# Kernel optimization log

Hardware: AMD Instinct MI355X
Metric: run time of the kernel (lower is better)

## Reference

```python
import jax, jax.numpy as jnp
import numpy as np

TAU = 1.0
LOSS_WEIGHT = 1.0
N = 4_000_000


def setup_inputs() -> dict:
    key = jax.random.key(0)
    k1, k2 = jax.random.split(key)

    def make_boxes(k):
        u = jax.random.uniform(k, (N, 5), dtype=jnp.float32)
        xy = u[:, :2] * 1024.0                 # centers in a 1024px image
        wh = u[:, 2:4] * 100.0 + 4.0           # box sizes in [4, 104)
        r = (u[:, 4:5] - 0.5) * jnp.pi         # angle in [-pi/2, pi/2)
        return jnp.concatenate([xy, wh, r], axis=-1)

    return {"pred": make_boxes(k1), "target": make_boxes(k2)}


def xy_wh_r_2_xy_sigma(xywhr):
    """(N,5) rbox -> (mu (N,2), sigma (N,2,2)) via R @ (S/2)^2 @ R^T closed form."""
    xy = xywhr[..., :2]
    wh = jnp.clip(xywhr[..., 2:4], 1e-7, 1e7)
    r = xywhr[..., 4]
    c, s = jnp.cos(r), jnp.sin(r)
    a = (0.5 * wh[..., 0]) ** 2  # (w/2)^2
    b = (0.5 * wh[..., 1]) ** 2  # (h/2)^2
    s00 = a * c * c + b * s * s
    s11 = a * s * s + b * c * c
    s01 = (a - b) * s * c
    sigma = jnp.stack(
        [jnp.stack([s00, s01], -1), jnp.stack([s01, s11], -1)], -2
    )  # (N,2,2)
    return xy, sigma


def _det2(m):
    return m[..., 0, 0] * m[..., 1, 1] - m[..., 0, 1] * m[..., 1, 0]


def _inv2(m):
    det = _det2(m)
    adj = jnp.stack(
        [jnp.stack([m[..., 1, 1], -m[..., 0, 1]], -1),
         jnp.stack([-m[..., 1, 0], m[..., 0, 0]], -1)], -2)
    return adj / det[..., None, None]


def kld_loss(mu_p, sigma_p, mu_t, sigma_t, tau):
    delta = mu_p - mu_t                                # (N,2)
    sigma_t_inv = _inv2(sigma_t)                       # (N,2,2)
    # delta^T Sigma_t^{-1} delta
    term1 = jnp.einsum('ni,nij,nj->n', delta, sigma_t_inv, delta)
    # tr(Sigma_t^{-1} Sigma_p) + log(det Sigma_t / det Sigma_p)
    tr = jnp.einsum('nij,nji->n', sigma_t_inv, sigma_p)
    term2 = tr + jnp.log(_det2(sigma_t) / _det2(sigma_p))
    dis = term1 + term2 - 2.0
    kl_dis = jnp.maximum(dis, 1e-6)
    # fun == 'log1p'
    loss = 1.0 - 1.0 / (tau + jnp.log1p(kl_dis))
    return loss[:, None]                               # (N,1) like torch version


def reference(pred, target):
    mu_p, sigma_p = xy_wh_r_2_xy_sigma(pred)
    mu_t, sigma_t = xy_wh_r_2_xy_sigma(target)
    return kld_loss(mu_p, sigma_p, mu_t, sigma_t, TAU) * LOSS_WEIGHT
```

## Files before the change

### kernel.cpp

```cpp
#include <hip/hip_runtime.h>
#include <math.h>

#define TAU_CONST 1.0f
#define BLOCK 256
#define RPT 4
#define RPB (BLOCK * RPT)
#define F4PB (RPB * 5 / 4)

__device__ __forceinline__ float fast_rcp(float x) { return __builtin_amdgcn_rcpf(x); }

__device__ __forceinline__ float kld_row(const float* p, const float* t) {
    float pw = fminf(fmaxf(p[2], 1e-7f), 1e7f), ph = fminf(fmaxf(p[3], 1e-7f), 1e7f);
    float tw = fminf(fmaxf(t[2], 1e-7f), 1e7f), th = fminf(fmaxf(t[3], 1e-7f), 1e7f);
    float ap = 0.25f * pw * pw, bp = 0.25f * ph * ph;
    float at = 0.25f * tw * tw, bt = 0.25f * th * th;
    float sp_, cp_; __sincosf(p[4], &sp_, &cp_);
    float st_, ct_; __sincosf(t[4], &st_, &ct_);
    float p00 = ap * cp_ * cp_ + bp * sp_ * sp_;
    float p11 = ap * sp_ * sp_ + bp * cp_ * cp_;
    float p01 = (ap - bp) * sp_ * cp_;
    float t00 = at * ct_ * ct_ + bt * st_ * st_;
    float t11 = at * st_ * st_ + bt * ct_ * ct_;
    float t01 = (at - bt) * st_ * ct_;
    float dp = p00 * p11 - p01 * p01;
    float dt = t00 * t11 - t01 * t01;
    float dx = p[0] - t[0], dy = p[1] - t[1];
    float inv_dt = fast_rcp(dt);
    float term1 = (dx * dx * t11 - 2.0f * dx * dy * t01 + dy * dy * t00) * inv_dt;
    float tr    = (t11 * p00 + t00 * p11 - 2.0f * t01 * p01) * inv_dt;
    float term2 = tr + (__logf(dt) - __logf(dp));
    float dis = term1 + term2 - 2.0f;
    float kl = fmaxf(dis, 1e-6f);
    return 1.0f - fast_rcp(TAU_CONST + __logf(1.0f + kl));
}

__global__ void __launch_bounds__(BLOCK) gdloss_lds_kernel(const float4* __restrict__ pred4,
                                                           const float4* __restrict__ targ4,
                                                           float4* __restrict__ out4,
                                                           int nf4_in, int n4_out) {
    __shared__ float4 sP[F4PB];
    __shared__ float4 sT[F4PB];
    const int tid = threadIdx.x;
    const int base4 = blockIdx.x * F4PB;
#pragma unroll
    for (int k = 0; k < 5; ++k) {
        int g = base4 + k * BLOCK + tid;
        float4 v, u;
        if (g < nf4_in) { v = pred4[g]; u = targ4[g]; }
        else            { v = float4{0, 0, 0, 0}; u = float4{0, 0, 0, 0}; }
        sP[k * BLOCK + tid] = v;
        sT[k * BLOCK + tid] = u;
    }
    __syncthreads();
    const float4* pRow = (const float4*)((const float*)sP + 20 * tid);
    const float4* tRow = (const float4*)((const float*)sT + 20 * tid);
    float4 lp[5], lt[5];
#pragma unroll
    for (int k = 0; k < 5; ++k) { lp[k] = pRow[k]; lt[k] = tRow[k]; }
    const float* P = (const float*)lp;
    const float* T = (const float*)lt;
    float4 o;
    o.x = kld_row(P + 0,  T + 0);
    o.y = kld_row(P + 5,  T + 5);
    o.z = kld_row(P + 10, T + 10);
    o.w = kld_row(P + 15, T + 15);
    int o4 = blockIdx.x * BLOCK + tid;
    if (o4 < n4_out) out4[o4] = o;
}

__global__ void gdloss_tail_kernel(const float* __restrict__ pred,
                                   const float* __restrict__ target,
                                   float* __restrict__ out, int start, int n) {
    int i = start + blockIdx.x * blockDim.x + threadIdx.x;
    if (i >= n) return;
    float p[5], t[5];
#pragma unroll
    for (int k = 0; k < 5; ++k) { p[k] = pred[5 * i + k]; t[k] = target[5 * i + k]; }
    out[i] = kld_row(p, t);
}

extern "C" void kernel_launch(void* const* d_in, const int* in_sizes, int n_in,
                              void* d_out, int out_size, void* d_ws, size_t ws_size,
                              hipStream_t stream) {
    const float* pred   = (const float*)d_in[0];
    const float* target = (const float*)d_in[1];
    float* out = (float*)d_out;
    const int n = in_sizes[0] / 5;
    const int n4 = n / 4;
    const int nf4_in = (n * 5) / 4;
    if (n4 > 0) {
        int blocks = (n4 + BLOCK - 1) / BLOCK;
        gdloss_lds_kernel<<<blocks, BLOCK, 0, stream>>>((const float4*)pred,
                                                        (const float4*)target,
                                                        (float4*)out, nf4_in, n4);
    }
    if (n - n4 * 4 > 0) {
        gdloss_tail_kernel<<<1, 64, 0, stream>>>(pred, target, out, n4 * 4, n);
    }
}
```

Baseline: 179.6 us.

## Replace LDS-staged kernel with grid-stride double-buffered register pipeline

Drops the shared-memory staging. Each thread now loads its own 4 rows (5 uncoalesced float4 per input) straight into registers. A persistent grid of at most 1024 blocks strides over the data and prefetches the next tile while computing the current one. Loads and stores use nontemporal hints. The direct per-thread loads stride 80 bytes across lanes, which loses coalescing, and the double buffers raise register pressure.

Result: slower. 194.4 us (+8.2%).

```diff
diff --git a/kernel.cpp b/kernel.cpp
--- a/kernel.cpp
+++ b/kernel.cpp
@@ -3,9 +3,9 @@
 
 #define TAU_CONST 1.0f
 #define BLOCK 256
-#define RPT 4
-#define RPB (BLOCK * RPT)
-#define F4PB (RPB * 5 / 4)
+#define NBLOCKS 1024
+
+typedef float vfloat4 __attribute__((ext_vector_type(4)));
 
 __device__ __forceinline__ float fast_rcp(float x) { return __builtin_amdgcn_rcpf(x); }
 
@@ -34,38 +34,63 @@
     return 1.0f - fast_rcp(TAU_CONST + __logf(1.0f + kl));
 }
 
-__global__ void __launch_bounds__(BLOCK) gdloss_lds_kernel(const float4* __restrict__ pred4,
-                                                           const float4* __restrict__ targ4,
-                                                           float4* __restrict__ out4,
-                                                           int nf4_in, int n4_out) {
-    __shared__ float4 sP[F4PB];
-    __shared__ float4 sT[F4PB];
-    const int tid = threadIdx.x;
-    const int base4 = blockIdx.x * F4PB;
+__device__ __forceinline__ void load_tile(const vfloat4* __restrict__ p4,
+                                          const vfloat4* __restrict__ t4,
+                                          int i, vfloat4* P, vfloat4* T) {
+    const long b = 5L * i;
 #pragma unroll
     for (int k = 0; k < 5; ++k) {
-        int g = base4 + k * BLOCK + tid;
-        float4 v, u;
-        if (g < nf4_in) { v = pred4[g]; u = targ4[g]; }
-        else            { v = float4{0, 0, 0, 0}; u = float4{0, 0, 0, 0}; }
-        sP[k * BLOCK + tid] = v;
-        sT[k * BLOCK + tid] = u;
+        P[k] = __builtin_nontemporal_load(p4 + b + k);
+        T[k] = __builtin_nontemporal_load(t4 + b + k);
     }
-    __syncthreads();
-    const float4* pRow = (const float4*)((const float*)sP + 20 * tid);
-    const float4* tRow = (const float4*)((const float*)sT + 20 * tid);
-    float4 lp[5], lt[5];
-#pragma unroll
-    for (int k = 0; k < 5; ++k) { lp[k] = pRow[k]; lt[k] = tRow[k]; }
-    const float* P = (const float*)lp;
-    const float* T = (const float*)lt;
-    float4 o;
-    o.x = kld_row(P + 0,  T + 0);
-    o.y = kld_row(P + 5,  T + 5);
-    o.z = kld_row(P + 10, T + 10);
-    o.w = kld_row(P + 15, T + 15);
-    int o4 = blockIdx.x * BLOCK + tid;
-    if (o4 < n4_out) out4[o4] = o;
+}
+
+__global__ void __launch_bounds__(BLOCK) gdloss_pipe_kernel(const vfloat4* __restrict__ pred4,
+                                                            const vfloat4* __restrict__ targ4,
+                                                            vfloat4* __restrict__ out4,
+                                                            int n4) {
+    const int stride = gridDim.x * blockDim.x;
+    int i = blockIdx.x * blockDim.x + threadIdx.x;
+    if (i >= n4) return;
+
+    vfloat4 Pa[5], Ta[5], Pb[5], Tb[5];
+    load_tile(pred4, targ4, i, Pa, Ta);
+
+    while (true) {
+        const int inext = i + stride;
+        const bool more = (inext < n4);
+        if (more) load_tile(pred4, targ4, inext, Pb, Tb);
+
+        {
+            const float* P = (const float*)Pa;
+            const float* T = (const float*)Ta;
+            vfloat4 o;
+            o.x = kld_row(P + 0,  T + 0);
+            o.y = kld_row(P + 5,  T + 5);
+            o.z = kld_row(P + 10, T + 10);
+            o.w = kld_row(P + 15, T + 15);
+            __builtin_nontemporal_store(o, out4 + i);
+        }
+        if (!more) break;
+        i = inext;
+
+        const int inext2 = i + stride;
+        const bool more2 = (inext2 < n4);
+        if (more2) load_tile(pred4, targ4, inext2, Pa, Ta);
+
+        {
+            const float* P = (const float*)Pb;
+            const float* T = (const float*)Tb;
+            vfloat4 o;
+            o.x = kld_row(P + 0,  T + 0);
+            o.y = kld_row(P + 5,  T + 5);
+            o.z = kld_row(P + 10, T + 10);
+            o.w = kld_row(P + 15, T + 15);
+            __builtin_nontemporal_store(o, out4 + i);
+        }
+        if (!more2) break;
+        i = inext2;
+    }
 }
 
 __global__ void gdloss_tail_kernel(const float* __restrict__ pred,
@@ -87,12 +112,12 @@
     float* out = (float*)d_out;
     const int n = in_sizes[0] / 5;
     const int n4 = n / 4;
-    const int nf4_in = (n * 5) / 4;
     if (n4 > 0) {
         int blocks = (n4 + BLOCK - 1) / BLOCK;
-        gdloss_lds_kernel<<<blocks, BLOCK, 0, stream>>>((const float4*)pred,
-                                                        (const float4*)target,
-                                                        (float4*)out, nf4_in, n4);
+        if (blocks > NBLOCKS) blocks = NBLOCKS;
+        gdloss_pipe_kernel<<<blocks, BLOCK, 0, stream>>>((const vfloat4*)pred,
+                                                         (const vfloat4*)target,
+                                                         (vfloat4*)out, n4);
     }
     if (n - n4 * 4 > 0) {
         gdloss_tail_kernel<<<1, 64, 0, stream>>>(pred, target, out, n4 * 4, n);
```

## Use double-angle closed form, hardware transcendentals, and direct per-thread float4 loads

Applied to the files above, without the earlier changes.

Rewrites the covariance build with double-angle identities and computes the determinants as a*b, so sin/cos of twice the angle come straight from the hardware sin/cos instructions, which take revolutions; r/pi gives revolutions for 2r. The two logs are merged into one hardware log2 of a ratio, cutting transcendental count. The LDS staging and barrier are dropped, and each thread reads its 5 float4s directly from global memory. Those reads are strided across the wavefront and rely on cache to coalesce, and the hardware sin/cos precision differs slightly from __sincosf.

Result: no change. 178.4 us (-0.6%).

```diff
diff --git a/kernel.cpp b/kernel.cpp
--- a/kernel.cpp
+++ b/kernel.cpp
@@ -3,69 +3,64 @@
 
 #define TAU_CONST 1.0f
 #define BLOCK 256
-#define RPT 4
-#define RPB (BLOCK * RPT)
-#define F4PB (RPB * 5 / 4)
+
+#define INV_PI 0.31830988618f
+#define LN2    0.69314718056f
 
 __device__ __forceinline__ float fast_rcp(float x) { return __builtin_amdgcn_rcpf(x); }
+__device__ __forceinline__ float fast_log2(float x) { return __builtin_amdgcn_logf(x); }
 
 __device__ __forceinline__ float kld_row(const float* p, const float* t) {
     float pw = fminf(fmaxf(p[2], 1e-7f), 1e7f), ph = fminf(fmaxf(p[3], 1e-7f), 1e7f);
     float tw = fminf(fmaxf(t[2], 1e-7f), 1e7f), th = fminf(fmaxf(t[3], 1e-7f), 1e7f);
     float ap = 0.25f * pw * pw, bp = 0.25f * ph * ph;
     float at = 0.25f * tw * tw, bt = 0.25f * th * th;
-    float sp_, cp_; __sincosf(p[4], &sp_, &cp_);
-    float st_, ct_; __sincosf(t[4], &st_, &ct_);
-    float p00 = ap * cp_ * cp_ + bp * sp_ * sp_;
-    float p11 = ap * sp_ * sp_ + bp * cp_ * cp_;
-    float p01 = (ap - bp) * sp_ * cp_;
-    float t00 = at * ct_ * ct_ + bt * st_ * st_;
-    float t11 = at * st_ * st_ + bt * ct_ * ct_;
-    float t01 = (at - bt) * st_ * ct_;
-    float dp = p00 * p11 - p01 * p01;
-    float dt = t00 * t11 - t01 * t01;
+
+    float revp = p[4] * INV_PI;
+    float revt = t[4] * INV_PI;
+    float s2p = __builtin_amdgcn_sinf(revp), c2p = __builtin_amdgcn_cosf(revp);
+    float s2t = __builtin_amdgcn_sinf(revt), c2t = __builtin_amdgcn_cosf(revt);
+
+    float hp = 0.5f * (ap + bp), qp = 0.5f * (ap - bp);
+    float ht = 0.5f * (at + bt), qt = 0.5f * (at - bt);
+    float p00 = hp + qp * c2p, p11 = hp - qp * c2p, p01 = qp * s2p;
+    float t00 = ht + qt * c2t, t11 = ht - qt * c2t, t01 = qt * s2t;
+
+    float dp = ap * bp;
+    float dt = at * bt;
+    float inv_dt = fast_rcp(dt);
+
     float dx = p[0] - t[0], dy = p[1] - t[1];
-    float inv_dt = fast_rcp(dt);
     float term1 = (dx * dx * t11 - 2.0f * dx * dy * t01 + dy * dy * t00) * inv_dt;
     float tr    = (t11 * p00 + t00 * p11 - 2.0f * t01 * p01) * inv_dt;
-    float term2 = tr + (__logf(dt) - __logf(dp));
-    float dis = term1 + term2 - 2.0f;
-    float kl = fmaxf(dis, 1e-6f);
-    return 1.0f - fast_rcp(TAU_CONST + __logf(1.0f + kl));
+    float logterm = LN2 * fast_log2(dt * fast_rcp(dp));
+
+    float dis = term1 + tr + logterm - 2.0f;
+    float kl  = fmaxf(dis, 1e-6f);
+    float denom = TAU_CONST + LN2 * fast_log2(1.0f + kl);
+    return 1.0f - fast_rcp(denom);
 }
 
-__global__ void __launch_bounds__(BLOCK) gdloss_lds_kernel(const float4* __restrict__ pred4,
-                                                           const float4* __restrict__ targ4,
-                                                           float4* __restrict__ out4,
-                                                           int nf4_in, int n4_out) {
-    __shared__ float4 sP[F4PB];
-    __shared__ float4 sT[F4PB];
-    const int tid = threadIdx.x;
-    const int base4 = blockIdx.x * F4PB;
+__global__ void __launch_bounds__(BLOCK) gdloss_hw_kernel(const float4* __restrict__ pred4,
+                                                          const float4* __restrict__ targ4,
+                                                          float4* __restrict__ out4, int n4) {
+    int tid = blockIdx.x * blockDim.x + threadIdx.x;
+    if (tid >= n4) return;
+    float4 pv[5], tv[5];
+    const long b = 5L * tid;
 #pragma unroll
     for (int k = 0; k < 5; ++k) {
-        int g = base4 + k * BLOCK + tid;
-        float4 v, u;
-        if (g < nf4_in) { v = pred4[g]; u = targ4[g]; }
-        else            { v = float4{0, 0, 0, 0}; u = float4{0, 0, 0, 0}; }
-        sP[k * BLOCK + tid] = v;
-        sT[k * BLOCK + tid] = u;
+        pv[k] = pred4[b + k];
+        tv[k] = targ4[b + k];
     }
-    __syncthreads();
-    const float4* pRow = (const float4*)((const float*)sP + 20 * tid);
-    const float4* tRow = (const float4*)((const float*)sT + 20 * tid);
-    float4 lp[5], lt[5];
-#pragma unroll
-    for (int k = 0; k < 5; ++k) { lp[k] = pRow[k]; lt[k] = tRow[k]; }
-    const float* P = (const float*)lp;
-    const float* T = (const float*)lt;
+    const float* P = (const float*)pv;
+    const float* T = (const float*)tv;
     float4 o;
     o.x = kld_row(P + 0,  T + 0);
     o.y = kld_row(P + 5,  T + 5);
     o.z = kld_row(P + 10, T + 10);
     o.w = kld_row(P + 15, T + 15);
-    int o4 = blockIdx.x * BLOCK + tid;
-    if (o4 < n4_out) out4[o4] = o;
+    out4[tid] = o;
 }
 
 __global__ void gdloss_tail_kernel(const float* __restrict__ pred,
@@ -87,12 +82,11 @@
     float* out = (float*)d_out;
     const int n = in_sizes[0] / 5;
     const int n4 = n / 4;
-    const int nf4_in = (n * 5) / 4;
     if (n4 > 0) {
         int blocks = (n4 + BLOCK - 1) / BLOCK;
-        gdloss_lds_kernel<<<blocks, BLOCK, 0, stream>>>((const float4*)pred,
-                                                        (const float4*)target,
-                                                        (float4*)out, nf4_in, n4);
+        gdloss_hw_kernel<<<blocks, BLOCK, 0, stream>>>((const float4*)pred,
+                                                       (const float4*)target,
+                                                       (float4*)out, n4);
     }
     if (n - n4 * 4 > 0) {
         gdloss_tail_kernel<<<1, 64, 0, stream>>>(pred, target, out, n4 * 4, n);
```
